# Optimization experiments

Hardware: AMD Instinct MI355X
Metric: run time of the kernel (lower is better)

## Reference

```python
import jax, jax.numpy as jnp
import numpy as np

N_NODES = 524288
N_EDGES = 786432
NUM_GRAPHS = 8192
NUM_NODE_TYPES = 16
NODE_DIM = 256
EDGE_DIM = 128
OUT_DIM = 1


def setup_inputs() -> dict:
    key = jax.random.key(0)
    ks = jax.random.split(key, 12)
    h_node = jax.random.uniform(ks[0], (N_NODES, NUM_NODE_TYPES), dtype=jnp.float32)
    pos_node = jax.random.normal(ks[1], (N_NODES, 3), dtype=jnp.float32)
    batch_node = jnp.sort(jax.random.randint(ks[2], (N_NODES,), 0, NUM_GRAPHS)).astype(jnp.int64)
    edge_index = jax.random.randint(ks[3], (2, N_EDGES), 0, N_NODES).astype(jnp.int64)
    batch_edge = jnp.sort(jax.random.randint(ks[4], (N_EDGES,), 0, NUM_GRAPHS)).astype(jnp.int64)
    s = 0.05
    W_node = jax.random.normal(ks[5], (NUM_NODE_TYPES, NODE_DIM), dtype=jnp.float32) * s
    W_edge = jax.random.normal(ks[6], (2 * NUM_NODE_TYPES, EDGE_DIM), dtype=jnp.float32) * s
    H = NODE_DIM + EDGE_DIM
    W1 = jax.random.normal(ks[7], (H, H), dtype=jnp.float32) * s
    b1 = jnp.zeros((H,), dtype=jnp.float32)
    W2 = jax.random.normal(ks[8], (H, OUT_DIM), dtype=jnp.float32) * s
    b2 = jnp.zeros((OUT_DIM,), dtype=jnp.float32)
    return {"h_node": h_node, "pos_node": pos_node, "batch_node": batch_node,
            "edge_index": edge_index, "batch_edge": batch_edge,
            "W_node": W_node, "W_edge": W_edge, "W1": W1, "b1": b1, "W2": W2, "b2": b2}


def _segment_mean(x, seg_ids, num_segments):
    # fused replacement for the original per-graph boolean-mask loop:
    # h[seg==k].mean(0) for all k, via one scatter-add + count normalize
    sums = jax.ops.segment_sum(x, seg_ids, num_segments=num_segments)
    cnts = jax.ops.segment_sum(jnp.ones((x.shape[0],), x.dtype), seg_ids, num_segments=num_segments)
    return sums / jnp.maximum(cnts, 1.0)[:, None]


def reference(h_node, pos_node, batch_node, edge_index, batch_edge,
              W_node, W_edge, W1, b1, W2, b2):
    # h_edge = cat(h_node[src], h_node[dst])  -> [E, 2*num_node_types]
    h_edge_raw = jnp.concatenate([h_node[edge_index[0]], h_node[edge_index[1]]], axis=-1)
    # num_timesteps == 0 path: plain embedders, no time embedding
    hn = h_node @ W_node          # [N, node_dim]
    he = h_edge_raw @ W_edge      # [E, edge_dim]
    # encoder treated as identity (NodeEdgeNet not in scope); pooling is the target op
    node_mean = _segment_mean(hn, batch_node, NUM_GRAPHS)  # [G, node_dim]
    edge_mean = _segment_mean(he, batch_edge, NUM_GRAPHS)  # [G, edge_dim]
    h_sub = jnp.concatenate([node_mean, edge_mean], axis=-1)  # [G, node_dim+edge_dim]
    # final MLP (num_layer=2): Linear -> ReLU -> Linear
    pred = jax.nn.relu(h_sub @ W1 + b1) @ W2 + b2  # [G, 1]
    return pred
```

## Files before the change

kernel.cpp:

```cpp
#include <hip/hip_runtime.h>

#define N_NODES_C   524288
#define N_EDGES_C   786432
#define NUM_GRAPHS_C 8192
#define NT 16
#define NODE_DIM_C 256
#define EDGE_DIM_C 128
#define HDIM 384
#define KC 48

#define WS_SN    0
#define WS_SE    65536
#define WS_NM    131072
#define WS_EM    655360
#define WS_WC    1703936

__device__ __forceinline__ int lower_bound_i32(const int* __restrict__ a, int n, int key) {
    int lo = 0, hi = n;
    while (lo < hi) {
        int mid = (lo + hi) >> 1;
        if (a[mid] < key) lo = mid + 1; else hi = mid;
    }
    return lo;
}

__global__ void k0_starts(const int* __restrict__ bnode, const int* __restrict__ bedge,
                          int* __restrict__ sn, int* __restrict__ se) {
    int t = blockIdx.x * blockDim.x + threadIdx.x;
    if (t < NUM_GRAPHS_C + 1) {
        sn[t] = lower_bound_i32(bnode, N_NODES_C, t);
    } else if (t < 2 * (NUM_GRAPHS_C + 1)) {
        int g = t - (NUM_GRAPHS_C + 1);
        se[g] = lower_bound_i32(bedge, N_EDGES_C, g);
    }
}

__global__ __launch_bounds__(HDIM) void kw_fold(
    const float* __restrict__ Wn, const float* __restrict__ We,
    const float* __restrict__ W1, float* __restrict__ Wc) {
    int k = blockIdx.x;
    int j = threadIdx.x;
    float acc = 0.f;
    if (k < NT) {
        const float* wr = &Wn[k * NODE_DIM_C];
        for (int kk = 0; kk < NODE_DIM_C; ++kk)
            acc = fmaf(wr[kk], W1[(size_t)kk * HDIM + j], acc);
    } else {
        const float* wr = &We[(k - NT) * EDGE_DIM_C];
        for (int kk = 0; kk < EDGE_DIM_C; ++kk)
            acc = fmaf(wr[kk], W1[(size_t)(NODE_DIM_C + kk) * HDIM + j], acc);
    }
    Wc[k * HDIM + j] = acc;
}

__device__ __forceinline__ void f4_shfl_xor_add(float4& a, int mask) {
    a.x += __shfl_xor(a.x, mask, 64);
    a.y += __shfl_xor(a.y, mask, 64);
    a.z += __shfl_xor(a.z, mask, 64);
    a.w += __shfl_xor(a.w, mask, 64);
}

__global__ __launch_bounds__(256) void k1_node_mean(
    const float* __restrict__ h_node, const int* __restrict__ sn,
    float* __restrict__ nm) {
    int wave = threadIdx.x >> 6;
    int lane = threadIdx.x & 63;
    int g = blockIdx.x * 4 + wave;
    int s = sn[g], e = sn[g + 1];
    int row_off = lane >> 2;
    int quad    = lane & 3;
    const float4* h4 = (const float4*)h_node;
    float4 acc = make_float4(0.f, 0.f, 0.f, 0.f);
    for (int i = s + row_off; i < e; i += 16) {
        float4 v = h4[(size_t)i * 4 + quad];
        acc.x += v.x; acc.y += v.y; acc.z += v.z; acc.w += v.w;
    }
    f4_shfl_xor_add(acc, 4);
    f4_shfl_xor_add(acc, 8);
    f4_shfl_xor_add(acc, 16);
    f4_shfl_xor_add(acc, 32);
    if (row_off == 0) {
        float inv = 1.f / fmaxf((float)(e - s), 1.f);
        float4 r = make_float4(acc.x * inv, acc.y * inv, acc.z * inv, acc.w * inv);
        ((float4*)nm)[(size_t)g * 4 + quad] = r;
    }
}

__global__ __launch_bounds__(256) void k2_edge_mean(
    const float* __restrict__ h_node,
    const int* __restrict__ esrc, const int* __restrict__ edst,
    const int* __restrict__ se, float* __restrict__ em) {
    int wave = threadIdx.x >> 6;
    int lane = threadIdx.x & 63;
    int g = blockIdx.x * 4 + wave;
    int s = se[g], e = se[g + 1];
    int e_off = lane >> 3;
    int p     = (lane >> 2) & 1;
    int quad  = lane & 3;
    const int* __restrict__ idxp = p ? edst : esrc;
    const float4* h4 = (const float4*)h_node;
    float4 acc = make_float4(0.f, 0.f, 0.f, 0.f);
    for (int i = s + e_off; i < e; i += 8) {
        int idx = idxp[i];
        float4 v = h4[(size_t)idx * 4 + quad];
        acc.x += v.x; acc.y += v.y; acc.z += v.z; acc.w += v.w;
    }
    f4_shfl_xor_add(acc, 8);
    f4_shfl_xor_add(acc, 16);
    f4_shfl_xor_add(acc, 32);
    if (e_off == 0) {
        float inv = 1.f / fmaxf((float)(e - s), 1.f);
        float4 r = make_float4(acc.x * inv, acc.y * inv, acc.z * inv, acc.w * inv);
        ((float4*)em)[(size_t)g * 8 + p * 4 + quad] = r;
    }
}

#define GPB 16
__global__ __launch_bounds__(HDIM) void k3_mlp(
    const float* __restrict__ nm, const float* __restrict__ em,
    const float* __restrict__ Wc, const float* __restrict__ b1,
    const float* __restrict__ W2, const float* __restrict__ b2,
    float* __restrict__ pred) {
    int j = threadIdx.x;
    float wc[KC];
    #pragma unroll
    for (int k = 0; k < KC; ++k) wc[k] = Wc[k * HDIM + j];
    float b1j = b1[j], w2j = W2[j], b20 = b2[0];

    __shared__ float fs[GPB][KC];
    __shared__ float part[GPB][6];
    int g0 = blockIdx.x * GPB;
    #pragma unroll
    for (int t = j; t < GPB * KC; t += HDIM) {
        int g = t / KC, k = t % KC;
        fs[g][k] = (k < NT) ? nm[(size_t)(g0 + g) * NT + k]
                            : em[(size_t)(g0 + g) * 32 + (k - NT)];
    }
    __syncthreads();

    int wave = j >> 6, lane = j & 63;
    for (int g = 0; g < GPB; ++g) {
        float z = b1j;
        #pragma unroll
        for (int k = 0; k < KC; ++k) z = fmaf(fs[g][k], wc[k], z);
        z = fmaxf(z, 0.f);
        float p = z * w2j;
        #pragma unroll
        for (int off = 32; off > 0; off >>= 1) p += __shfl_down(p, off, 64);
        if (lane == 0) part[g][wave] = p;
    }
    __syncthreads();
    if (j < GPB) {
        float sacc = b20;
        #pragma unroll
        for (int w = 0; w < 6; ++w) sacc += part[j][w];
        pred[g0 + j] = sacc;
    }
}

extern "C" void kernel_launch(void* const* d_in, const int* in_sizes, int n_in,
                              void* d_out, int out_size, void* d_ws, size_t ws_size,
                              hipStream_t stream) {
    const float* h_node     = (const float*)d_in[0];
    const int*   batch_node = (const int*)d_in[2];
    const int*   edge_index = (const int*)d_in[3];
    const int*   batch_edge = (const int*)d_in[4];
    const float* W_node     = (const float*)d_in[5];
    const float* W_edge     = (const float*)d_in[6];
    const float* W1         = (const float*)d_in[7];
    const float* b1         = (const float*)d_in[8];
    const float* W2         = (const float*)d_in[9];
    const float* b2         = (const float*)d_in[10];
    float* pred = (float*)d_out;

    char* ws = (char*)d_ws;
    int*   sn = (int*)(ws + WS_SN);
    int*   se = (int*)(ws + WS_SE);
    float* nm = (float*)(ws + WS_NM);
    float* em = (float*)(ws + WS_EM);
    float* Wc = (float*)(ws + WS_WC);

    const int* esrc = edge_index;
    const int* edst = edge_index + N_EDGES_C;

    kw_fold<<<KC, HDIM, 0, stream>>>(W_node, W_edge, W1, Wc);
    {
        int total = 2 * (NUM_GRAPHS_C + 1);
        k0_starts<<<(total + 255) / 256, 256, 0, stream>>>(batch_node, batch_edge, sn, se);
    }
    k1_node_mean<<<NUM_GRAPHS_C / 4, 256, 0, stream>>>(h_node, sn, nm);
    k2_edge_mean<<<NUM_GRAPHS_C / 4, 256, 0, stream>>>(h_node, esrc, edst, se, em);
    k3_mlp<<<NUM_GRAPHS_C / GPB, HDIM, 0, stream>>>(nm, em, Wc, b1, W2, b2, pred);
}
```

Baseline: 175.7 us.

## Merge prep and mean kernels into fewer launches, unroll edge gather

Merges the segment-start search and the weight fold into one kernel whose block ranges do different jobs. Also merges the node-mean and edge-mean kernels into a single launch split by block index. The edge gather loop now handles two edges per iteration with separate accumulators so more loads are in flight. This cuts launch overhead and lets the node and edge passes run on the GPU at the same time, at the cost of some branch divergence across blocks.

Measured after the change: 161.8 us. 1.09x faster.

```diff
diff --git a/kernel.cpp b/kernel.cpp
--- a/kernel.cpp
+++ b/kernel.cpp
@@ -9,6 +9,9 @@
 #define HDIM 384
 #define KC 48
 
+#define START_BLOCKS 65
+#define FOLD_BLOCKS  72
+
 #define WS_SN    0
 #define WS_SE    65536
 #define WS_NM    131072
@@ -24,33 +27,37 @@
     return lo;
 }
 
-__global__ void k0_starts(const int* __restrict__ bnode, const int* __restrict__ bedge,
-                          int* __restrict__ sn, int* __restrict__ se) {
-    int t = blockIdx.x * blockDim.x + threadIdx.x;
-    if (t < NUM_GRAPHS_C + 1) {
-        sn[t] = lower_bound_i32(bnode, N_NODES_C, t);
-    } else if (t < 2 * (NUM_GRAPHS_C + 1)) {
-        int g = t - (NUM_GRAPHS_C + 1);
-        se[g] = lower_bound_i32(bedge, N_EDGES_C, g);
-    }
-}
-
-__global__ __launch_bounds__(HDIM) void kw_fold(
+__global__ __launch_bounds__(256) void kp_prep(
+    const int* __restrict__ bnode, const int* __restrict__ bedge,
     const float* __restrict__ Wn, const float* __restrict__ We,
-    const float* __restrict__ W1, float* __restrict__ Wc) {
-    int k = blockIdx.x;
-    int j = threadIdx.x;
-    float acc = 0.f;
-    if (k < NT) {
-        const float* wr = &Wn[k * NODE_DIM_C];
-        for (int kk = 0; kk < NODE_DIM_C; ++kk)
-            acc = fmaf(wr[kk], W1[(size_t)kk * HDIM + j], acc);
+    const float* __restrict__ W1,
+    int* __restrict__ sn, int* __restrict__ se, float* __restrict__ Wc) {
+    int blk = blockIdx.x;
+    if (blk < START_BLOCKS) {
+        int t = blk * 256 + threadIdx.x;
+        if (t < NUM_GRAPHS_C + 1) {
+            sn[t] = lower_bound_i32(bnode, N_NODES_C, t);
+        } else if (t < 2 * (NUM_GRAPHS_C + 1)) {
+            se[t - (NUM_GRAPHS_C + 1)] = lower_bound_i32(bedge, N_EDGES_C, t - (NUM_GRAPHS_C + 1));
+        }
     } else {
-        const float* wr = &We[(k - NT) * EDGE_DIM_C];
-        for (int kk = 0; kk < EDGE_DIM_C; ++kk)
-            acc = fmaf(wr[kk], W1[(size_t)(NODE_DIM_C + kk) * HDIM + j], acc);
-    }
-    Wc[k * HDIM + j] = acc;
+        int o = (blk - START_BLOCKS) * 256 + threadIdx.x;
+        if (o >= KC * HDIM) return;
+        int k = o / HDIM, j = o % HDIM;
+        float acc = 0.f;
+        if (k < NT) {
+            const float* wr = &Wn[k * NODE_DIM_C];
+            #pragma unroll 4
+            for (int kk = 0; kk < NODE_DIM_C; ++kk)
+                acc = fmaf(wr[kk], W1[(size_t)kk * HDIM + j], acc);
+        } else {
+            const float* wr = &We[(k - NT) * EDGE_DIM_C];
+            #pragma unroll 4
+            for (int kk = 0; kk < EDGE_DIM_C; ++kk)
+                acc = fmaf(wr[kk], W1[(size_t)(NODE_DIM_C + kk) * HDIM + j], acc);
+        }
+        Wc[o] = acc;
+    }
 }
 
 __device__ __forceinline__ void f4_shfl_xor_add(float4& a, int mask) {
@@ -60,58 +67,65 @@
     a.w += __shfl_xor(a.w, mask, 64);
 }
 
-__global__ __launch_bounds__(256) void k1_node_mean(
+__global__ __launch_bounds__(256) void km_means(
     const float* __restrict__ h_node, const int* __restrict__ sn,
-    float* __restrict__ nm) {
+    const int* __restrict__ se,
+    const int* __restrict__ esrc, const int* __restrict__ edst,
+    float* __restrict__ nm, float* __restrict__ em) {
     int wave = threadIdx.x >> 6;
     int lane = threadIdx.x & 63;
-    int g = blockIdx.x * 4 + wave;
-    int s = sn[g], e = sn[g + 1];
-    int row_off = lane >> 2;
-    int quad    = lane & 3;
     const float4* h4 = (const float4*)h_node;
-    float4 acc = make_float4(0.f, 0.f, 0.f, 0.f);
-    for (int i = s + row_off; i < e; i += 16) {
-        float4 v = h4[(size_t)i * 4 + quad];
-        acc.x += v.x; acc.y += v.y; acc.z += v.z; acc.w += v.w;
-    }
-    f4_shfl_xor_add(acc, 4);
-    f4_shfl_xor_add(acc, 8);
-    f4_shfl_xor_add(acc, 16);
-    f4_shfl_xor_add(acc, 32);
-    if (row_off == 0) {
-        float inv = 1.f / fmaxf((float)(e - s), 1.f);
-        float4 r = make_float4(acc.x * inv, acc.y * inv, acc.z * inv, acc.w * inv);
-        ((float4*)nm)[(size_t)g * 4 + quad] = r;
-    }
-}
-
-__global__ __launch_bounds__(256) void k2_edge_mean(
-    const float* __restrict__ h_node,
-    const int* __restrict__ esrc, const int* __restrict__ edst,
-    const int* __restrict__ se, float* __restrict__ em) {
-    int wave = threadIdx.x >> 6;
-    int lane = threadIdx.x & 63;
-    int g = blockIdx.x * 4 + wave;
-    int s = se[g], e = se[g + 1];
-    int e_off = lane >> 3;
-    int p     = (lane >> 2) & 1;
-    int quad  = lane & 3;
-    const int* __restrict__ idxp = p ? edst : esrc;
-    const float4* h4 = (const float4*)h_node;
-    float4 acc = make_float4(0.f, 0.f, 0.f, 0.f);
-    for (int i = s + e_off; i < e; i += 8) {
-        int idx = idxp[i];
-        float4 v = h4[(size_t)idx * 4 + quad];
-        acc.x += v.x; acc.y += v.y; acc.z += v.z; acc.w += v.w;
-    }
-    f4_shfl_xor_add(acc, 8);
-    f4_shfl_xor_add(acc, 16);
-    f4_shfl_xor_add(acc, 32);
-    if (e_off == 0) {
-        float inv = 1.f / fmaxf((float)(e - s), 1.f);
-        float4 r = make_float4(acc.x * inv, acc.y * inv, acc.z * inv, acc.w * inv);
-        ((float4*)em)[(size_t)g * 8 + p * 4 + quad] = r;
+
+    if (blockIdx.x < 2048) {
+        int g = blockIdx.x * 4 + wave;
+        int s = sn[g], e = sn[g + 1];
+        int row_off = lane >> 2;
+        int quad    = lane & 3;
+        float4 acc = make_float4(0.f, 0.f, 0.f, 0.f);
+        for (int i = s + row_off; i < e; i += 16) {
+            float4 v = h4[(size_t)i * 4 + quad];
+            acc.x += v.x; acc.y += v.y; acc.z += v.z; acc.w += v.w;
+        }
+        f4_shfl_xor_add(acc, 4);
+        f4_shfl_xor_add(acc, 8);
+        f4_shfl_xor_add(acc, 16);
+        f4_shfl_xor_add(acc, 32);
+        if (row_off == 0) {
+            float inv = 1.f / fmaxf((float)(e - s), 1.f);
+            ((float4*)nm)[(size_t)g * 4 + quad] =
+                make_float4(acc.x * inv, acc.y * inv, acc.z * inv, acc.w * inv);
+        }
+    } else {
+        int g = (blockIdx.x - 2048) * 4 + wave;
+        int s = se[g], e = se[g + 1];
+        int e_off = lane >> 3;
+        int p     = (lane >> 2) & 1;
+        int quad  = lane & 3;
+        const int* __restrict__ idxp = p ? edst : esrc;
+        float4 acc0 = make_float4(0.f, 0.f, 0.f, 0.f);
+        float4 acc1 = make_float4(0.f, 0.f, 0.f, 0.f);
+        int i = s + e_off;
+        for (; i + 8 < e; i += 16) {
+            int ia = idxp[i];
+            int ib = idxp[i + 8];
+            float4 va = h4[(size_t)ia * 4 + quad];
+            float4 vb = h4[(size_t)ib * 4 + quad];
+            acc0.x += va.x; acc0.y += va.y; acc0.z += va.z; acc0.w += va.w;
+            acc1.x += vb.x; acc1.y += vb.y; acc1.z += vb.z; acc1.w += vb.w;
+        }
+        if (i < e) {
+            float4 v = h4[(size_t)idxp[i] * 4 + quad];
+            acc0.x += v.x; acc0.y += v.y; acc0.z += v.z; acc0.w += v.w;
+        }
+        acc0.x += acc1.x; acc0.y += acc1.y; acc0.z += acc1.z; acc0.w += acc1.w;
+        f4_shfl_xor_add(acc0, 8);
+        f4_shfl_xor_add(acc0, 16);
+        f4_shfl_xor_add(acc0, 32);
+        if (e_off == 0) {
+            float inv = 1.f / fmaxf((float)(e - s), 1.f);
+            ((float4*)em)[(size_t)g * 8 + p * 4 + quad] =
+                make_float4(acc0.x * inv, acc0.y * inv, acc0.z * inv, acc0.w * inv);
+        }
     }
 }
 
@@ -183,12 +197,8 @@
     const int* esrc = edge_index;
     const int* edst = edge_index + N_EDGES_C;
 
-    kw_fold<<<KC, HDIM, 0, stream>>>(W_node, W_edge, W1, Wc);
-    {
-        int total = 2 * (NUM_GRAPHS_C + 1);
-        k0_starts<<<(total + 255) / 256, 256, 0, stream>>>(batch_node, batch_edge, sn, se);
-    }
-    k1_node_mean<<<NUM_GRAPHS_C / 4, 256, 0, stream>>>(h_node, sn, nm);
-    k2_edge_mean<<<NUM_GRAPHS_C / 4, 256, 0, stream>>>(h_node, esrc, edst, se, em);
+    kp_prep<<<START_BLOCKS + FOLD_BLOCKS, 256, 0, stream>>>(
+        batch_node, batch_edge, W_node, W_edge, W1, sn, se, Wc);
+    km_means<<<4096, 256, 0, stream>>>(h_node, sn, se, esrc, edst, nm, em);
     k3_mlp<<<NUM_GRAPHS_C / GPB, HDIM, 0, stream>>>(nm, em, Wc, b1, W2, b2, pred);
 }
```
